# Kernel optimization log

Measured on AMD Instinct MI355X. Metric: run time of the kernel, lower is better.

The kernel has to match this reference:

```python
import jax, jax.numpy as jnp
import numpy as np

INP = 64   # inplanes
PLN = 64   # planes
LOC = 64   # loc_planes
EPS = 1e-5


def _linear_init(key, fan_in, fan_out):
    # torch nn.Linear default: U(-1/sqrt(fan_in), 1/sqrt(fan_in)) for W and b
    kw, kb = jax.random.split(key)
    bound = 1.0 / np.sqrt(fan_in)
    W = jax.random.uniform(kw, (fan_in, fan_out), jnp.float32, -bound, bound)
    b = jax.random.uniform(kb, (fan_out,), jnp.float32, -bound, bound)
    return W, b


def setup_inputs() -> dict:
    key = jax.random.key(0)
    ks = jax.random.split(key, 8)
    B, N = 8, 4096
    img_fea = jax.random.normal(ks[0], (B, N, INP), jnp.float32)
    loc_fea = jax.random.normal(ks[1], (B, N, LOC), jnp.float32)
    W11, b11 = _linear_init(ks[2], INP + LOC, INP)
    W12, b12 = _linear_init(ks[3], INP, INP)
    W21, b21 = _linear_init(ks[4], INP + LOC, INP)
    W22, b22 = _linear_init(ks[5], INP, INP * PLN)
    W3, b3 = _linear_init(ks[6], PLN, PLN)
    ln_g = jnp.ones((PLN,), jnp.float32)
    ln_b = jnp.zeros((PLN,), jnp.float32)
    return {
        "img_fea": img_fea, "loc_fea": loc_fea,
        "W11": W11, "b11": b11, "W12": W12, "b12": b12,
        "W21": W21, "b21": b21, "W22": W22, "b22": b22,
        "ln_g": ln_g, "ln_b": ln_b, "W3": W3, "b3": b3,
    }


def reference(img_fea, loc_fea, W11, b11, W12, b12, W21, b21, W22, b22,
              ln_g, ln_b, W3, b3):
    B, N, C = img_fea.shape
    cat_fea = jnp.concatenate([img_fea, loc_fea], axis=2)  # [B,N,INP+LOC]
    # branch 1: per-token input vector
    w11 = jax.nn.relu(cat_fea @ W11 + b11)                 # [B,N,INP]
    w12 = w11 @ W12 + b12                                  # [B,N,INP]
    # branch 2: per-token weight matrix generation
    w21 = jax.nn.relu(cat_fea @ W21 + b21)                 # [B,N,INP]
    w22 = (w21 @ W22 + b22).reshape(B, N, INP, PLN)        # [B,N,INP,PLN]
    # batched tiny matvec: (1,INP) @ (INP,PLN) per token
    x = jnp.einsum('bni,bnio->bno', w12, w22)              # [B,N,PLN]
    # LayerNorm over last dim + ReLU
    mu = jnp.mean(x, axis=-1, keepdims=True)
    var = jnp.mean(jnp.square(x - mu), axis=-1, keepdims=True)
    x = (x - mu) * jax.lax.rsqrt(var + EPS) * ln_g + ln_b
    x = jax.nn.relu(x)
    # final linear (no activation)
    return x @ W3 + b3
```

## Files before the change

### kernel.cpp

```cpp
#include <hip/hip_runtime.h>
#include <cstdint>


typedef __bf16 bf16x4 __attribute__((ext_vector_type(4)));
typedef __bf16 bf16x8 __attribute__((ext_vector_type(8)));
typedef float  f32x4  __attribute__((ext_vector_type(4)));

#define MFMA16(A, B, C) __builtin_amdgcn_mfma_f32_16x16x32_bf16(A, B, C, 0, 0, 0)

#define SYNC_PIPE(N) asm volatile("s_waitcnt vmcnt(" #N ")\n\ts_barrier" ::: "memory")

#define OFF_BT22 0
#define OFF_W11  266240
#define OFF_W21  274432
#define OFF_W12  282624
#define OFF_W3   286720

__global__ __launch_bounds__(256) void prep_kernel(
    const float* __restrict__ W22, const float* __restrict__ b22,
    const float* __restrict__ W11, const float* __restrict__ W21,
    const float* __restrict__ W12, const float* __restrict__ W3,
    __bf16* __restrict__ ws)
{
    __shared__ __bf16 T[64][72];
    const int b = blockIdx.x, tid = threadIdx.x;
    const float* src; __bf16* dst;
    if (b < 64)       { src = W22 + b * 4096;        dst = ws + OFF_BT22 + b * 4096; }
    else if (b == 64) { src = b22;                   dst = ws + OFF_BT22 + 64 * 4096; }
    else if (b < 67)  { src = W11 + (b - 65) * 4096; dst = ws + OFF_W11 + (b - 65) * 4096; }
    else if (b < 69)  { src = W21 + (b - 67) * 4096; dst = ws + OFF_W21 + (b - 67) * 4096; }
    else if (b == 69) { src = W12;                   dst = ws + OFF_W12; }
    else              { src = W3;                    dst = ws + OFF_W3; }
    #pragma unroll
    for (int it = 0; it < 4; ++it) {
        int u = it * 1024 + tid * 4;
        int r = u >> 6, c = u & 63;
        const float4 v = *(const float4*)(src + u);
        T[r][c] = (__bf16)v.x; T[r][c + 1] = (__bf16)v.y;
        T[r][c + 2] = (__bf16)v.z; T[r][c + 3] = (__bf16)v.w;
    }
    __syncthreads();
    #pragma unroll
    for (int it = 0; it < 2; ++it) {
        int item = it * 256 + tid;
        int q = item >> 6, o = item & 63;
        bf16x8 pk;
        #pragma unroll
        for (int kj = 0; kj < 8; ++kj) pk[kj] = T[q * 8 + kj][o];
        *(bf16x8*)(dst + q * 512 + o * 8) = pk;
    }
}

__global__ __launch_bounds__(256, 2) void main_kernel(
    const float* __restrict__ img, const float* __restrict__ loc,
    const float* __restrict__ b11, const float* __restrict__ b12,
    const float* __restrict__ b21, const float* __restrict__ ln_g,
    const float* __restrict__ ln_b, const float* __restrict__ b3,
    const __bf16* __restrict__ ws, float* __restrict__ out)
{
    __shared__ __align__(1024) char smem[57856];
    __bf16* catL = (__bf16*)smem;
    __bf16* w11L = (__bf16*)(smem + 17920);
    __bf16* w12L = (__bf16*)(smem + 27648);
    float2* ps   = (float2*)smem;
    __bf16* xL   = (__bf16*)(smem + 4096);
    __bf16* w21T = (__bf16*)(smem + 49152);

    const int tid  = threadIdx.x;
    const int wv   = tid >> 6;
    const int lane = tid & 63;
    const int ln   = lane & 15;
    const int quad = lane >> 4;
    const int ob   = wv * 16;
    const long tb  = (long)blockIdx.x * 64;

    const __bf16* Bt22  = ws + OFF_BT22;
    const __bf16* W11bt = ws + OFF_W11;
    const __bf16* W21bt = ws + OFF_W21;
    const __bf16* W12bt = ws + OFF_W12;
    const __bf16* W3bt  = ws + OFF_W3;

    {
        const float* srcs[2] = {img, loc};
        #pragma unroll
        for (int s = 0; s < 2; ++s) {
            const float* src = srcs[s] + tb * 64;
            #pragma unroll
            for (int it = 0; it < 4; ++it) {
                int u = (it * 256 + tid) * 4;
                int t = u >> 6, c = u & 63;
                const float4 v = *(const float4*)(src + u);
                bf16x4 pk = {(__bf16)v.x, (__bf16)v.y, (__bf16)v.z, (__bf16)v.w};
                *(bf16x4*)(catL + t * 136 + s * 64 + c) = pk;
            }
        }
    }
    __syncthreads();

    {
        const int isW21 = wv >> 1;
        const int cb0 = (wv & 1) * 32;
        const __bf16* Wbt = isW21 ? W21bt : W11bt;
        const float* bsel = isW21 ? b21 : b11;
        f32x4 a1[4][2] = {};
        #pragma unroll
        for (int kb = 0; kb < 4; ++kb) {
            bf16x8 af[4];
            #pragma unroll
            for (int mf = 0; mf < 4; ++mf)
                af[mf] = *(const bf16x8*)(catL + (mf*16 + ln)*136 + kb*32 + quad*8);
            #pragma unroll
            for (int nf = 0; nf < 2; ++nf) {
                bf16x8 bw = *(const bf16x8*)(Wbt + ((kb*4 + quad)*64 + cb0 + nf*16 + ln)*8);
                #pragma unroll
                for (int mf = 0; mf < 4; ++mf)
                    a1[mf][nf] = MFMA16(af[mf], bw, a1[mf][nf]);
            }
        }
        if (!isW21) {
            #pragma unroll
            for (int nf = 0; nf < 2; ++nf) {
                int o = cb0 + nf*16 + ln;
                float cb = bsel[o];
                #pragma unroll
                for (int mf = 0; mf < 4; ++mf)
                    #pragma unroll
                    for (int r = 0; r < 4; ++r) {
                        int t = mf*16 + quad*4 + r;
                        float v = a1[mf][nf][r] + cb; v = v > 0.f ? v : 0.f;
                        w11L[t*72 + o] = (__bf16)v;
                    }
            }
        } else {
            #pragma unroll
            for (int nf = 0; nf < 2; ++nf) {
                int o = cb0 + nf*16 + ln;
                float cb = bsel[o];
                #pragma unroll
                for (int mf = 0; mf < 4; ++mf) {
                    bf16x4 pk;
                    #pragma unroll
                    for (int r = 0; r < 4; ++r) {
                        float v = a1[mf][nf][r] + cb; v = v > 0.f ? v : 0.f;
                        pk[r] = (__bf16)v;
                    }
                    *(bf16x4*)(w21T + o*68 + mf*16 + quad*4) = pk;
                }
            }
        }
    }
    __syncthreads();

    {
        float c12 = b12[ob + ln];
        f32x4 a12c[4] = {};
        #pragma unroll
        for (int kb = 0; kb < 2; ++kb) {
            bf16x8 af[4];
            #pragma unroll
            for (int mf = 0; mf < 4; ++mf)
                af[mf] = *(const bf16x8*)(w11L + (mf*16 + ln)*72 + kb*32 + quad*8);
            bf16x8 bw = *(const bf16x8*)(W12bt + ((kb*4 + quad)*64 + ob + ln)*8);
            #pragma unroll
            for (int mf = 0; mf < 4; ++mf)
                a12c[mf] = MFMA16(af[mf], bw, a12c[mf]);
        }
        #pragma unroll
        for (int mf = 0; mf < 4; ++mf)
            #pragma unroll
            for (int r = 0; r < 4; ++r) {
                int t = mf*16 + quad*4 + r;
                w12L[t*72 + ob + ln] = (__bf16)(a12c[mf][r] + c12);
            }
    }
    __syncthreads();

    bf16x8 a12[4][2];
    #pragma unroll
    for (int mf = 0; mf < 4; ++mf)
        #pragma unroll
        for (int sub = 0; sub < 2; ++sub)
            a12[mf][sub] = *(const bf16x8*)(w12L + (mf*16 + ln)*72 + sub*32 + quad*8);
    __syncthreads();

    auto stage = [&](int c) {
        const int ng = (c == 32) ? 8 : 16;
        char* buf = smem + (c % 3) * 16384;
        for (int g = wv; g < ng; g += 4) {
            const __bf16* gsrc = Bt22 + ((long)c * 8192 + g * 512) + lane * 8;
            void* ldst = buf + g * 1024;
            __builtin_amdgcn_global_load_lds(
                (const __attribute__((address_space(1))) uint32_t*)gsrc,
                (__attribute__((address_space(3))) uint32_t*)ldst, 16, 0, 0);
        }
    };
    stage(0); stage(1);
    SYNC_PIPE(4);

    f32x4 acc[4] = {};
    for (int c = 0; c <= 32; ++c) {
        if (c <= 30) stage(c + 2);
        const __bf16* buf = (const __bf16*)(smem + (c % 3) * 16384);
        if (c < 32) {
            #pragma unroll
            for (int jj = 0; jj < 2; ++jj) {
                const int j = c*2 + jj;
                f32x4 w4[4];
                #pragma unroll
                for (int mf = 0; mf < 4; ++mf) {
                    bf16x4 wv4 = *(const bf16x4*)(w21T + j*68 + mf*16 + quad*4);
                    w4[mf] = __builtin_convertvector(wv4, f32x4);
                }
                bf16x8 bf0 = *(const bf16x8*)(buf + (jj*8     + quad)*512 + (ob + ln)*8);
                bf16x8 bf1 = *(const bf16x8*)(buf + (jj*8 + 4 + quad)*512 + (ob + ln)*8);
                #pragma unroll
                for (int mf = 0; mf < 4; ++mf) {
                    f32x4 fz = {};
                    f32x4 m = MFMA16(a12[mf][0], bf0, fz);
                    m = MFMA16(a12[mf][1], bf1, m);
                    #pragma unroll
                    for (int r = 0; r < 4; ++r)
                        acc[mf][r] = fmaf(w4[mf][r], m[r], acc[mf][r]);
                }
            }
        } else {
            #pragma unroll
            for (int sub = 0; sub < 2; ++sub) {
                bf16x8 bfr = *(const bf16x8*)(buf + (sub*4 + quad)*512 + (ob + ln)*8);
                #pragma unroll
                for (int mf = 0; mf < 4; ++mf)
                    acc[mf] = MFMA16(a12[mf][sub], bfr, acc[mf]);
            }
        }
        if (c <= 29)      SYNC_PIPE(4);
        else if (c == 30) SYNC_PIPE(2);
        else if (c == 31) SYNC_PIPE(0);
    }

    #pragma unroll
    for (int mf = 0; mf < 4; ++mf)
        #pragma unroll
        for (int r = 0; r < 4; ++r) {
            float v = acc[mf][r];
            float s1 = v, s2 = v*v;
            #pragma unroll
            for (int d = 1; d < 16; d <<= 1) {
                s1 += __shfl_xor(s1, d, 64);
                s2 += __shfl_xor(s2, d, 64);
            }
            if (ln == 0) {
                int t = mf*16 + quad*4 + r;
                ps[t*4 + wv] = make_float2(s1, s2);
            }
        }
    __syncthreads();

    float gv = ln_g[ob + ln], bv = ln_b[ob + ln], b3v = b3[ob + ln];
    #pragma unroll
    for (int mf = 0; mf < 4; ++mf)
        #pragma unroll
        for (int r = 0; r < 4; ++r) {
            int t = mf*16 + quad*4 + r;
            float2 p0 = ps[t*4], p1 = ps[t*4 + 1], p2 = ps[t*4 + 2], p3 = ps[t*4 + 3];
            float mean = (p0.x + p1.x + p2.x + p3.x) * 0.015625f;
            float var  = (p0.y + p1.y + p2.y + p3.y) * 0.015625f - mean * mean;
            float inv  = rsqrtf(var + 1e-5f);
            float v = (acc[mf][r] - mean) * inv * gv + bv;
            v = v > 0.f ? v : 0.f;
            xL[t*72 + ob + ln] = (__bf16)v;
        }
    __syncthreads();

    f32x4 a3[4] = {};
    #pragma unroll
    for (int kb = 0; kb < 2; ++kb) {
        bf16x8 af[4];
        #pragma unroll
        for (int mf = 0; mf < 4; ++mf)
            af[mf] = *(const bf16x8*)(xL + (mf*16 + ln)*72 + kb*32 + quad*8);
        bf16x8 bfr = *(const bf16x8*)(W3bt + ((kb*4 + quad)*64 + ob + ln)*8);
        #pragma unroll
        for (int mf = 0; mf < 4; ++mf)
            a3[mf] = MFMA16(af[mf], bfr, a3[mf]);
    }
    #pragma unroll
    for (int mf = 0; mf < 4; ++mf)
        #pragma unroll
        for (int r = 0; r < 4; ++r) {
            long t = tb + mf*16 + quad*4 + r;
            out[t*64 + ob + ln] = a3[mf][r] + b3v;
        }
}

extern "C" void kernel_launch(void* const* d_in, const int* in_sizes, int n_in,
                              void* d_out, int out_size, void* d_ws, size_t ws_size,
                              hipStream_t stream)
{
    const float* img  = (const float*)d_in[0];
    const float* loc  = (const float*)d_in[1];
    const float* W11  = (const float*)d_in[2];
    const float* b11  = (const float*)d_in[3];
    const float* W12  = (const float*)d_in[4];
    const float* b12  = (const float*)d_in[5];
    const float* W21  = (const float*)d_in[6];
    const float* b21  = (const float*)d_in[7];
    const float* W22  = (const float*)d_in[8];
    const float* b22  = (const float*)d_in[9];
    const float* ln_g = (const float*)d_in[10];
    const float* ln_b = (const float*)d_in[11];
    const float* W3   = (const float*)d_in[12];
    const float* b3   = (const float*)d_in[13];
    __bf16* ws = (__bf16*)d_ws;
    float*  o  = (float*)d_out;

    prep_kernel<<<71, 256, 0, stream>>>(W22, b22, W11, W21, W12, W3, ws);
    main_kernel<<<512, 256, 0, stream>>>(img, loc, b11, b12, b21, ln_g, ln_b, b3, ws, o);
}
```

Measured before the change: 127.7 us.

## Load W22 fragments directly into registers with wave-private layout instead of LDS staging

```diff
diff --git a/kernel.cpp b/kernel.cpp
--- a/kernel.cpp
+++ b/kernel.cpp
@@ -7,8 +7,6 @@
 typedef float  f32x4  __attribute__((ext_vector_type(4)));
 
 #define MFMA16(A, B, C) __builtin_amdgcn_mfma_f32_16x16x32_bf16(A, B, C, 0, 0, 0)
-
-#define SYNC_PIPE(N) asm volatile("s_waitcnt vmcnt(" #N ")\n\ts_barrier" ::: "memory")
 
 #define OFF_BT22 0
 #define OFF_W11  266240
@@ -24,13 +22,13 @@
 {
     __shared__ __bf16 T[64][72];
     const int b = blockIdx.x, tid = threadIdx.x;
-    const float* src; __bf16* dst;
-    if (b < 64)       { src = W22 + b * 4096;        dst = ws + OFF_BT22 + b * 4096; }
-    else if (b == 64) { src = b22;                   dst = ws + OFF_BT22 + 64 * 4096; }
-    else if (b < 67)  { src = W11 + (b - 65) * 4096; dst = ws + OFF_W11 + (b - 65) * 4096; }
-    else if (b < 69)  { src = W21 + (b - 67) * 4096; dst = ws + OFF_W21 + (b - 67) * 4096; }
-    else if (b == 69) { src = W12;                   dst = ws + OFF_W12; }
-    else              { src = W3;                    dst = ws + OFF_W3; }
+    const float* src; long base = 0;
+    if (b < 64)       { src = W22 + b * 4096; }
+    else if (b == 64) { src = b22; }
+    else if (b < 67)  { src = W11 + (b - 65) * 4096; base = OFF_W11 + (b - 65) * 4096; }
+    else if (b < 69)  { src = W21 + (b - 67) * 4096; base = OFF_W21 + (b - 67) * 4096; }
+    else if (b == 69) { src = W12;                   base = OFF_W12; }
+    else              { src = W3;                    base = OFF_W3; }
     #pragma unroll
     for (int it = 0; it < 4; ++it) {
         int u = it * 1024 + tid * 4;
@@ -47,7 +45,14 @@
         bf16x8 pk;
         #pragma unroll
         for (int kj = 0; kj < 8; ++kj) pk[kj] = T[q * 8 + kj][o];
-        *(bf16x8*)(dst + q * 512 + o * 8) = pk;
+        long dstE;
+        if (b <= 64) {
+            int k8 = (b == 64 ? 512 : b * 8) + q;
+            dstE = OFF_BT22 + ((long)(o >> 4) * 520 + k8) * 128 + (o & 15) * 8;
+        } else {
+            dstE = base + q * 512 + o * 8;
+        }
+        *(bf16x8*)(ws + dstE) = pk;
     }
 }
 
@@ -58,13 +63,13 @@
     const float* __restrict__ ln_b, const float* __restrict__ b3,
     const __bf16* __restrict__ ws, float* __restrict__ out)
 {
-    __shared__ __align__(1024) char smem[57856];
+    __shared__ __align__(1024) char smem[46592];
     __bf16* catL = (__bf16*)smem;
-    __bf16* w11L = (__bf16*)(smem + 17920);
-    __bf16* w12L = (__bf16*)(smem + 27648);
-    float2* ps   = (float2*)smem;
-    __bf16* xL   = (__bf16*)(smem + 4096);
-    __bf16* w21T = (__bf16*)(smem + 49152);
+    __bf16* w11L = (__bf16*)(smem + 17408);
+    __bf16* w12L = (__bf16*)(smem + 26624);
+    __bf16* w21T = (__bf16*)(smem + 35840);
+    float2* ps   = (float2*)(smem + 44544);
+    __bf16* xL   = w11L;
 
     const int tid  = threadIdx.x;
     const int wv   = tid >> 6;
@@ -181,61 +186,59 @@
         #pragma unroll
         for (int sub = 0; sub < 2; ++sub)
             a12[mf][sub] = *(const bf16x8*)(w12L + (mf*16 + ln)*72 + sub*32 + quad*8);
-    __syncthreads();
-
-    auto stage = [&](int c) {
-        const int ng = (c == 32) ? 8 : 16;
-        char* buf = smem + (c % 3) * 16384;
-        for (int g = wv; g < ng; g += 4) {
-            const __bf16* gsrc = Bt22 + ((long)c * 8192 + g * 512) + lane * 8;
-            void* ldst = buf + g * 1024;
-            __builtin_amdgcn_global_load_lds(
-                (const __attribute__((address_space(1))) uint32_t*)gsrc,
-                (__attribute__((address_space(3))) uint32_t*)ldst, 16, 0, 0);
-        }
+
+    const __bf16* Bw = Bt22 + ((long)wv * 520 + quad) * 128 + ln * 8;
+    auto loadch = [&](bf16x8* dst, int c) {
+        #pragma unroll
+        for (int s = 0; s < 4; ++s)
+            dst[s] = *(const bf16x8*)(Bw + (c*16 + s*4) * 128);
     };
-    stage(0); stage(1);
-    SYNC_PIPE(4);
+    bf16x8 biasb[2];
+    #pragma unroll
+    for (int s = 0; s < 2; ++s)
+        biasb[s] = *(const bf16x8*)(Bw + (512 + s*4) * 128);
 
     f32x4 acc[4] = {};
-    for (int c = 0; c <= 32; ++c) {
-        if (c <= 30) stage(c + 2);
-        const __bf16* buf = (const __bf16*)(smem + (c % 3) * 16384);
-        if (c < 32) {
-            #pragma unroll
-            for (int jj = 0; jj < 2; ++jj) {
-                const int j = c*2 + jj;
-                f32x4 w4[4];
+    auto compute = [&](const bf16x8* buf, int c) {
+        #pragma unroll
+        for (int jj = 0; jj < 2; ++jj) {
+            const int j = c*2 + jj;
+            f32x4 w4[4];
+            #pragma unroll
+            for (int mf = 0; mf < 4; ++mf) {
+                bf16x4 wv4 = *(const bf16x4*)(w21T + j*68 + mf*16 + quad*4);
+                w4[mf] = __builtin_convertvector(wv4, f32x4);
+            }
+            #pragma unroll
+            for (int mf = 0; mf < 4; ++mf) {
+                f32x4 fz = {};
+                f32x4 m = MFMA16(a12[mf][0], buf[jj*2],     fz);
+                m       = MFMA16(a12[mf][1], buf[jj*2 + 1], m);
                 #pragma unroll
-                for (int mf = 0; mf < 4; ++mf) {
-                    bf16x4 wv4 = *(const bf16x4*)(w21T + j*68 + mf*16 + quad*4);
-                    w4[mf] = __builtin_convertvector(wv4, f32x4);
-                }
-                bf16x8 bf0 = *(const bf16x8*)(buf + (jj*8     + quad)*512 + (ob + ln)*8);
-                bf16x8 bf1 = *(const bf16x8*)(buf + (jj*8 + 4 + quad)*512 + (ob + ln)*8);
-                #pragma unroll
-                for (int mf = 0; mf < 4; ++mf) {
-                    f32x4 fz = {};
-                    f32x4 m = MFMA16(a12[mf][0], bf0, fz);
-                    m = MFMA16(a12[mf][1], bf1, m);
-                    #pragma unroll
-                    for (int r = 0; r < 4; ++r)
-                        acc[mf][r] = fmaf(w4[mf][r], m[r], acc[mf][r]);
-                }
-            }
-        } else {
-            #pragma unroll
-            for (int sub = 0; sub < 2; ++sub) {
-                bf16x8 bfr = *(const bf16x8*)(buf + (sub*4 + quad)*512 + (ob + ln)*8);
-                #pragma unroll
-                for (int mf = 0; mf < 4; ++mf)
-                    acc[mf] = MFMA16(a12[mf][sub], bfr, acc[mf]);
-            }
-        }
-        if (c <= 29)      SYNC_PIPE(4);
-        else if (c == 30) SYNC_PIPE(2);
-        else if (c == 31) SYNC_PIPE(0);
-    }
+                for (int r = 0; r < 4; ++r)
+                    acc[mf][r] = fmaf(w4[mf][r], m[r], acc[mf][r]);
+            }
+        }
+    };
+
+    bf16x8 B0[4], B1[4], B2[4], B3[4];
+    loadch(B0, 0); loadch(B1, 1);
+    #pragma unroll 1
+    for (int cc = 0; cc < 32; cc += 4) {
+        loadch(B2, cc + 2);
+        compute(B0, cc);
+        loadch(B3, cc + 3);
+        compute(B1, cc + 1);
+        if (cc + 4 < 32) loadch(B0, cc + 4);
+        compute(B2, cc + 2);
+        if (cc + 5 < 32) loadch(B1, cc + 5);
+        compute(B3, cc + 3);
+    }
+    #pragma unroll
+    for (int s = 0; s < 2; ++s)
+        #pragma unroll
+        for (int mf = 0; mf < 4; ++mf)
+            acc[mf] = MFMA16(a12[mf][s], biasb[s], acc[mf]);
 
     #pragma unroll
     for (int mf = 0; mf < 4; ++mf)
```

Measured after the change: 153.1 us. 1.2x slower.
